# Kernel tuning notes

Measured on AMD Instinct MI355X. Metric: run time of the kernel, lower is better.

## Reference

```python
import jax, jax.numpy as jnp
import numpy as np

B, T = 1, 1024
V, C, H, L = 50304, 768, 12, 6
K = C // H              # 64, d_head
F = int(C * 3.5) // 32 * 32   # 2688, d_ffn
GN_EPS = 6.4e-4


def _layernorm(x, wb, eps=1e-5):
    mu = x.mean(-1, keepdims=True)
    var = jnp.var(x, axis=-1, keepdims=True)
    return (x - mu) * jax.lax.rsqrt(var + eps) * wb[0] + wb[1]


def _groupnorm(x, wb):  # x: [N, C], groups of size K per head
    xg = x.reshape(-1, H, K)
    mu = xg.mean(-1, keepdims=True)
    var = jnp.var(xg, axis=-1, keepdims=True)
    xg = (xg - mu) * jax.lax.rsqrt(var + GN_EPS)
    return xg.reshape(-1, C) * wb[0] + wb[1]


def _lerp(a, b, w):  # torch.lerp(a, b, w) = a + (b - a) * w
    return a + (b - a) * w


def _shift(x):  # token-shift with zero initial state (fresh LayerState)
    return jnp.concatenate([jnp.zeros_like(x[:, :1]), x[:, :-1]], axis=1)


def _layer(x, p):
    (tm_ln, tm_ts, Wr, Wk, Wv, Wg, Wo, bonus, decay, tm_gn,
     cm_ln, cm_ts, Win, Wout, cWg) = p
    # ---- time mixer ----
    xn = _layernorm(x, tm_ln)
    xp = _shift(xn)
    r = (_lerp(xp, xn, tm_ts[0]) @ Wr).reshape(B, T, H, K)
    k = (_lerp(xp, xn, tm_ts[1]) @ Wk).reshape(B, T, H, K)
    v = (_lerp(xp, xn, tm_ts[2]) @ Wv).reshape(B, T, H, K)
    g = _lerp(xp, xn, tm_ts[3]) @ Wg
    w = jnp.exp(-jnp.exp(decay))  # [H, K] per-channel decay

    def wkv_step(kv, rkv):  # kv: [B,H,K,V]
        r_t, k_t, v_t = rkv  # each [B,H,K]
        a = k_t[..., :, None] * v_t[..., None, :]          # outer product kv_t
        out = jnp.einsum('bhk,bhkv->bhv', r_t, kv + a * bonus[..., None])
        return kv * w[..., None] + a, out

    kv0 = jnp.zeros((B, H, K, K), x.dtype)
    kv_final, out = jax.lax.scan(
        wkv_step, kv0,
        (r.transpose(1, 0, 2, 3), k.transpose(1, 0, 2, 3),
         v.transpose(1, 0, 2, 3)))
    out = out.transpose(1, 0, 2, 3).reshape(B, T, C)
    out = _groupnorm(out.reshape(B * T, C), tm_gn).reshape(B, T, C)
    x = x + (out * jax.nn.silu(g)) @ Wo
    # ---- channel mixer ----
    xn = _layernorm(x, cm_ln)
    xp = _shift(xn)
    h = jnp.square(jax.nn.relu(_lerp(xp, xn, cm_ts[0]) @ Win))
    x = x + (h @ Wout) * jax.nn.sigmoid(_lerp(xp, xn, cm_ts[1]) @ cWg)
    return x, kv_final


def _forward(tokens, embed, embed_ln, tm_ln, tm_ts, tm_Wr, tm_Wk, tm_Wv,
             tm_Wg, tm_Wo, tm_bonus, tm_decay, tm_gn, cm_ln, cm_ts, cm_Win,
             cm_Wout, cm_Wg, head_ln, unembed):
    x = _layernorm(embed[tokens], embed_ln)
    stacked = (tm_ln, tm_ts, tm_Wr, tm_Wk, tm_Wv, tm_Wg, tm_Wo, tm_bonus,
               tm_decay, tm_gn, cm_ln, cm_ts, cm_Win, cm_Wout, cm_Wg)
    x, _ = jax.lax.scan(_layer, x, stacked)  # scan over the L layers
    return _layernorm(x, head_ln) @ unembed  # logits [B, T, V]


def setup_inputs() -> dict:
    key = jax.random.key(0)
    ks = iter(jax.random.split(key, 48))

    def rn(shape, s=0.02):
        return s * jax.random.normal(next(ks), shape, jnp.float32)

    def ln(pre=()):  # stacked (weight, bias) of a LayerNorm/GroupNorm
        return jnp.stack([1.0 + rn(pre + (C,)), rn(pre + (C,))], axis=len(pre))

    return {
        'tokens': jax.random.randint(next(ks), (B, T), 0, V),
        'embed': rn((V, C)),
        'embed_ln': ln(),
        'tm_ln': ln((L,)),
        'tm_ts': jax.random.uniform(next(ks), (L, 4, C), jnp.float32),
        'tm_Wr': rn((L, C, C)),
        'tm_Wk': rn((L, C, C)),
        'tm_Wv': rn((L, C, C)),
        'tm_Wg': rn((L, C, C)),
        'tm_Wo': rn((L, C, C)),
        'tm_bonus': rn((L, H, K), 0.5),
        'tm_decay': rn((L, H, K), 0.5),
        'tm_gn': ln((L,)),
        'cm_ln': ln((L,)),
        'cm_ts': jax.random.uniform(next(ks), (L, 2, C), jnp.float32),
        'cm_Win': rn((L, C, F)),
        'cm_Wout': rn((L, F, C)),
        'cm_Wg': rn((L, C, C)),
        'head_ln': ln(),
        'unembed': rn((C, V)),
    }


def reference(tokens, embed, embed_ln, tm_ln, tm_ts, tm_Wr, tm_Wk, tm_Wv,
              tm_Wg, tm_Wo, tm_bonus, tm_decay, tm_gn, cm_ln, cm_ts, cm_Win,
              cm_Wout, cm_Wg, head_ln, unembed):
    return _forward(tokens, embed, embed_ln, tm_ln, tm_ts, tm_Wr, tm_Wk,
                    tm_Wv, tm_Wg, tm_Wo, tm_bonus, tm_decay, tm_gn, cm_ln,
                    cm_ts, cm_Win, cm_Wout, cm_Wg, head_ln, unembed)
```

## Files before the change

kernel.cpp:

```cpp
#include <hip/hip_runtime.h>
#include <hip/hip_bf16.h>

#define T_LEN 1024
#define CDIM  768
#define HNUM  12
#define KDIM  64
#define LNUM  6
#define FDIM  2688
#define VDIM  50304
#define NCH   16
#define LCH   64

#define WSZ   (CDIM * CDIM)
#define WIN_OFF  (6 * WSZ)
#define WOUT_OFF (WIN_OFF + CDIM * FDIM)
#define WBUF_ELEMS (WOUT_OFF + FDIM * CDIM)

typedef __attribute__((ext_vector_type(4))) float f32x4;
typedef __attribute__((ext_vector_type(8))) short s16x8;

__device__ __forceinline__ ushort f2bf(float f) {
    union { float fv; unsigned u; } v; v.fv = f;
    unsigned r = v.u + 0x7fffu + ((v.u >> 16) & 1u);
    return (ushort)(r >> 16);
}

__device__ __forceinline__ void gload_lds16(const ushort* g, ushort* l) {
    __builtin_amdgcn_global_load_lds(
        (const __attribute__((address_space(1))) void*)g,
        (__attribute__((address_space(3))) void*)l, 16, 0, 0);
}

template <int N_>
__device__ __forceinline__ void wait_vm() {
    if constexpr (N_ == 0)      asm volatile("s_waitcnt vmcnt(0)" ::: "memory");
    else if constexpr (N_ == 4) asm volatile("s_waitcnt vmcnt(4)" ::: "memory");
    else if constexpr (N_ == 6) asm volatile("s_waitcnt vmcnt(6)" ::: "memory");
    else if constexpr (N_ == 8) asm volatile("s_waitcnt vmcnt(8)" ::: "memory");
    else                        asm volatile("s_waitcnt vmcnt(12)" ::: "memory");
}
__device__ __forceinline__ void barrier_asm() {
    asm volatile("s_barrier" ::: "memory");
}

__device__ __forceinline__ void trans_tile(const float* __restrict__ in,
        ushort* __restrict__ out, int R, int C, int tk, int tn) {
    __shared__ float tile[64][65];
    int tid = threadIdx.x;
    int r = tid >> 4, c4 = (tid & 15) << 2;
    int k0 = tk << 6, n0 = tn << 6;
    #pragma unroll
    for (int j = 0; j < 4; j++) {
        int rr = r + j * 16;
        float4 f = *(const float4*)&in[(size_t)(k0 + rr) * C + n0 + c4];
        tile[rr][c4 + 0] = f.x; tile[rr][c4 + 1] = f.y;
        tile[rr][c4 + 2] = f.z; tile[rr][c4 + 3] = f.w;
    }
    __syncthreads();
    #pragma unroll
    for (int j = 0; j < 4; j++) {
        int n = r + j * 16;
        ushort4 u;
        u.x = f2bf(tile[c4 + 0][n]);
        u.y = f2bf(tile[c4 + 1][n]);
        u.z = f2bf(tile[c4 + 2][n]);
        u.w = f2bf(tile[c4 + 3][n]);
        *(ushort4*)&out[(size_t)(n0 + n) * R + k0 + c4] = u;
    }
}

__global__ __launch_bounds__(256)
void k_trans(const float* __restrict__ in, ushort* __restrict__ out, int R, int C) {
    trans_tile(in, out, R, C, blockIdx.y, blockIdx.x);
}

__device__ __forceinline__ void conv_layer_tile(int t,
        const float* p0, const float* p1, const float* p2, const float* p3,
        const float* p4, const float* p5, const float* pWin, const float* pWout,
        ushort* wl) {
    const float* in; ushort* out; int R, C, tk, tn;
    if (t < 864) {
        int mi = t / 144, tt = t % 144;
        switch (mi) {
            case 0: in = p0; break; case 1: in = p1; break;
            case 2: in = p2; break; case 3: in = p3; break;
            case 4: in = p4; break; default: in = p5; break;
        }
        out = wl + (size_t)mi * WSZ; R = 768; C = 768;
        tk = tt / 12; tn = tt % 12;
    } else if (t < 1368) {
        int tt = t - 864;
        in = pWin; out = wl + WIN_OFF; R = 768; C = 2688;
        tk = tt / 42; tn = tt % 42;
    } else {
        int tt = t - 1368;
        in = pWout; out = wl + WOUT_OFF; R = 2688; C = 768;
        tk = tt / 12; tn = tt % 12;
    }
    trans_tile(in, out, R, C, tk, tn);
}

__global__ __launch_bounds__(256)
void k_conv_layer(const float* p0, const float* p1, const float* p2,
                  const float* p3, const float* p4, const float* p5,
                  const float* pWin, const float* pWout, ushort* wl) {
    conv_layer_tile(blockIdx.x, p0, p1, p2, p3, p4, p5, pWin, pWout, wl);
}

__global__ __launch_bounds__(256)
void k_conv_all(const float* Wr, const float* Wk, const float* Wv,
                const float* Wg, const float* Wo, const float* Wcg,
                const float* Win, const float* Wout, const float* unemb,
                ushort* wbuf, ushort* ubuf) {
    int b = blockIdx.x;
    if (b < 6 * 1872) {
        int l = b / 1872, t = b % 1872;
        conv_layer_tile(t,
            Wr + (size_t)l * WSZ, Wk + (size_t)l * WSZ, Wv + (size_t)l * WSZ,
            Wg + (size_t)l * WSZ, Wo + (size_t)l * WSZ, Wcg + (size_t)l * WSZ,
            Win + (size_t)l * CDIM * FDIM, Wout + (size_t)l * FDIM * CDIM,
            wbuf + (size_t)l * WBUF_ELEMS);
    } else {
        int t = b - 6 * 1872;
        int tk = t / 786, tn = t % 786;
        trans_tile(unemb, ubuf, CDIM, VDIM, tk, tn);
    }
}

__global__ __launch_bounds__(256)
void k_ln_bf(const float* __restrict__ x, const float* __restrict__ wb,
             ushort* __restrict__ out) {
    int t = blockIdx.x, tid = threadIdx.x;
    float v[3]; float s = 0.f, s2 = 0.f;
    #pragma unroll
    for (int j = 0; j < 3; j++) {
        v[j] = x[(size_t)t * CDIM + tid + j * 256];
        s += v[j]; s2 += v[j] * v[j];
    }
    #pragma unroll
    for (int m = 32; m; m >>= 1) { s += __shfl_xor(s, m); s2 += __shfl_xor(s2, m); }
    __shared__ float rs[4], rq[4];
    int w = tid >> 6;
    if ((tid & 63) == 0) { rs[w] = s; rq[w] = s2; }
    __syncthreads();
    s = rs[0] + rs[1] + rs[2] + rs[3];
    s2 = rq[0] + rq[1] + rq[2] + rq[3];
    float mu = s * (1.f / CDIM);
    float inv = rsqrtf(s2 * (1.f / CDIM) - mu * mu + 1e-5f);
    #pragma unroll
    for (int j = 0; j < 3; j++) {
        int c = tid + j * 256;
        out[(size_t)t * CDIM + c] = f2bf((v[j] - mu) * inv * wb[c] + wb[CDIM + c]);
    }
}

__global__ __launch_bounds__(256)
void k_embed_ln(const int* __restrict__ tok, const float* __restrict__ embed,
                const float* __restrict__ wb, float* __restrict__ xout) {
    int t = blockIdx.x, tid = threadIdx.x;
    const float* row = embed + (size_t)tok[t] * CDIM;
    float v[3]; float s = 0.f, s2 = 0.f;
    #pragma unroll
    for (int j = 0; j < 3; j++) {
        v[j] = row[tid + j * 256]; s += v[j]; s2 += v[j] * v[j];
    }
    #pragma unroll
    for (int m = 32; m; m >>= 1) { s += __shfl_xor(s, m); s2 += __shfl_xor(s2, m); }
    __shared__ float rs[4], rq[4];
    int w = tid >> 6;
    if ((tid & 63) == 0) { rs[w] = s; rq[w] = s2; }
    __syncthreads();
    s = rs[0] + rs[1] + rs[2] + rs[3];
    s2 = rq[0] + rq[1] + rq[2] + rq[3];
    float mu = s * (1.f / CDIM);
    float inv = rsqrtf(s2 * (1.f / CDIM) - mu * mu + 1e-5f);
    #pragma unroll
    for (int j = 0; j < 3; j++) {
        int c = tid + j * 256;
        xout[(size_t)t * CDIM + c] = (v[j] - mu) * inv * wb[c] + wb[CDIM + c];
    }
}

template <int NM>
__global__ __launch_bounds__(256)
void k_lnlerp(const float* __restrict__ x, const float* __restrict__ lnw,
              const float* __restrict__ ts, ushort* __restrict__ mix) {
    int t = blockIdx.x, tid = threadIdx.x;
    bool has = (t > 0);
    float vb[3], va[3];
    float sb = 0.f, qb = 0.f, sa = 0.f, qa = 0.f;
    #pragma unroll
    for (int j = 0; j < 3; j++) {
        int c = tid + j * 256;
        vb[j] = x[(size_t)t * CDIM + c];
        sb += vb[j]; qb += vb[j] * vb[j];
        va[j] = has ? x[(size_t)(t - 1) * CDIM + c] : 0.f;
        sa += va[j]; qa += va[j] * va[j];
    }
    #pragma unroll
    for (int m = 32; m; m >>= 1) {
        sb += __shfl_xor(sb, m); qb += __shfl_xor(qb, m);
        sa += __shfl_xor(sa, m); qa += __shfl_xor(qa, m);
    }
    __shared__ float r0[4], r1[4], r2[4], r3[4];
    int w = tid >> 6;
    if ((tid & 63) == 0) { r0[w] = sb; r1[w] = qb; r2[w] = sa; r3[w] = qa; }
    __syncthreads();
    sb = r0[0] + r0[1] + r0[2] + r0[3]; qb = r1[0] + r1[1] + r1[2] + r1[3];
    sa = r2[0] + r2[1] + r2[2] + r2[3]; qa = r3[0] + r3[1] + r3[2] + r3[3];
    float mub = sb * (1.f / CDIM);
    float invb = rsqrtf(qb * (1.f / CDIM) - mub * mub + 1e-5f);
    float mua = sa * (1.f / CDIM);
    float inva = rsqrtf(qa * (1.f / CDIM) - mua * mua + 1e-5f);
    #pragma unroll
    for (int j = 0; j < 3; j++) {
        int c = tid + j * 256;
        float wgt = lnw[c], bia = lnw[CDIM + c];
        float xb = (vb[j] - mub) * invb * wgt + bia;
        float xa = has ? (va[j] - mua) * inva * wgt + bia : 0.f;
        #pragma unroll
        for (int m = 0; m < NM; m++) {
            float tv = ts[m * CDIM + c];
            mix[((size_t)m * T_LEN + t) * CDIM + c] = f2bf(xa + (xb - xa) * tv);
        }
    }
}

template <int BM, int BN, int EPI>
__device__ __forceinline__ void gemm_body(
        const ushort* __restrict__ A, const ushort* __restrict__ Bt,
        float* __restrict__ Cf, ushort* __restrict__ Cb,
        const float* __restrict__ resid, const float* __restrict__ gate,
        int N, int K, int mb, int nb, ushort* Al, ushort* Bl) {
    const int tid = threadIdx.x, lane = tid & 63, wave = tid >> 6;
    constexpr int WM = BM / 2, WN = BN / 2, FM = WM / 16, FN = WN / 16;
    const int wm = (wave >> 1) * WM, wn = (wave & 1) * WN;
    constexpr int AR = (BM * 8) / 256;
    constexpr int BR = (BN * 8) / 256;
    constexpr int LD = AR + BR;

    auto stage = [&](int buf, int kt) {
        int k0 = kt << 6;
        #pragma unroll
        for (int r = 0; r < AR; r++) {
            int slot = tid + r * 256;
            int row = slot >> 3, g = slot & 7;
            int gk = ((g ^ (row & 7)) << 3);
            gload_lds16(A + (size_t)(mb + row) * K + k0 + gk,
                        &Al[buf * BM * 64 + slot * 8]);
        }
        #pragma unroll
        for (int r = 0; r < BR; r++) {
            int slot = tid + r * 256;
            int row = slot >> 3, g = slot & 7;
            int gk = ((g ^ (row & 7)) << 3);
            gload_lds16(Bt + (size_t)(nb + row) * K + k0 + gk,
                        &Bl[buf * BN * 64 + slot * 8]);
        }
    };

    f32x4 acc[FM][FN];
    #pragma unroll
    for (int i = 0; i < FM; i++)
        #pragma unroll
        for (int j = 0; j < FN; j++) acc[i][j] = (f32x4)0.f;

    const int nt = K >> 6;
    stage(0, 0);
    stage(1, 1);
    int cur = 0;
    for (int t = 0; t < nt; t++) {
        if (t + 1 < nt) wait_vm<LD>();
        else            wait_vm<0>();
        barrier_asm();
        const ushort* Ab = &Al[cur * BM * 64];
        const ushort* Bb = &Bl[cur * BN * 64];
        const int kq = lane >> 4, ln15 = lane & 15;
        #pragma unroll
        for (int s = 0; s < 2; s++) {
            s16x8 af[FM], bfr[FN];
            #pragma unroll
            for (int i = 0; i < FM; i++) {
                int row = wm + i * 16 + ln15;
                int g = (s * 4 + kq) ^ (row & 7);
                af[i] = *(const s16x8*)&Ab[row * 64 + g * 8];
            }
            #pragma unroll
            for (int j = 0; j < FN; j++) {
                int row = wn + j * 16 + ln15;
                int g = (s * 4 + kq) ^ (row & 7);
                bfr[j] = *(const s16x8*)&Bb[row * 64 + g * 8];
            }
            #pragma unroll
            for (int i = 0; i < FM; i++)
                #pragma unroll
                for (int j = 0; j < FN; j++)
                    acc[i][j] = __builtin_amdgcn_mfma_f32_16x16x32_bf16(
                        af[i], bfr[j], acc[i][j], 0, 0, 0);
        }
        barrier_asm();
        if (t + 2 < nt) stage(cur, t + 2);
        cur ^= 1;
    }
    #pragma unroll
    for (int i = 0; i < FM; i++) {
        int rbase = mb + wm + i * 16 + (lane >> 4) * 4;
        #pragma unroll
        for (int j = 0; j < FN; j++) {
            int col = nb + wn + j * 16 + (lane & 15);
            #pragma unroll
            for (int r = 0; r < 4; r++) {
                size_t idx = (size_t)(rbase + r) * N + col;
                float vv = acc[i][j][r];
                if constexpr (EPI == 0) {
                    Cf[idx] = vv;
                } else if constexpr (EPI == 1) {
                    Cf[idx] = resid[idx] + vv;
                } else if constexpr (EPI == 2) {
                    float z = vv > 0.f ? vv * vv : 0.f;
                    Cb[idx] = f2bf(z);
                } else {
                    float gv = gate[idx];
                    Cf[idx] = resid[idx] + vv / (1.f + __expf(-gv));
                }
            }
        }
    }
}

template <int BM, int BN, int EPI, bool BATCH>
__global__ __launch_bounds__(256)
void k_gemm_std(const ushort* __restrict__ A, const ushort* __restrict__ Bt,
                float* __restrict__ Cf, ushort* __restrict__ Cb,
                const float* __restrict__ resid, const float* __restrict__ gate,
                int N, int K) {
    __shared__ __align__(16) ushort Al[2 * BM * 64];
    __shared__ __align__(16) ushort Bl[2 * BN * 64];
    if constexpr (BATCH) {
        int z = blockIdx.z;
        A  += (size_t)z * T_LEN * CDIM;
        Bt += (size_t)z * CDIM * CDIM;
        Cf += (size_t)z * T_LEN * CDIM;
    }
    gemm_body<BM, BN, EPI>(A, Bt, Cf, Cb, resid, gate, N, K,
                           blockIdx.y * BM, blockIdx.x * BN, Al, Bl);
}

__global__ __launch_bounds__(256)
void k_gemm_head(const ushort* __restrict__ A, const ushort* __restrict__ Bt,
                 float* __restrict__ C) {
    __shared__ __align__(16) ushort Al[2 * 128 * 64];
    __shared__ __align__(16) ushort Bl[2 * 128 * 64];
    int id = blockIdx.x;
    int xcd = id & 7, slot = id >> 3;
    int mb = slot & 7, nbl = slot >> 3;
    int nb = nbl * 8 + xcd;
    if (nb >= VDIM / 128) return;
    gemm_body<128, 128, 0>(A, Bt, C, nullptr, nullptr, nullptr,
                           VDIM, CDIM, mb * 128, nb * 128, Al, Bl);
}

__global__ __launch_bounds__(256)
void k_cmix(const ushort* __restrict__ mix, const ushort* __restrict__ wl,
            ushort* __restrict__ hb, float* __restrict__ gcm) {
    __shared__ __align__(16) ushort Al[2 * 128 * 64];
    __shared__ __align__(16) ushort Bl[2 * 64 * 64];
    int bx = blockIdx.x, mb = blockIdx.y * 128;
    if (bx < FDIM / 64) {
        gemm_body<128, 64, 2>(mix, wl + WIN_OFF, nullptr, hb, nullptr, nullptr,
                              FDIM, CDIM, mb, bx * 64, Al, Bl);
    } else {
        gemm_body<128, 64, 0>(mix + (size_t)T_LEN * CDIM, wl + 5 * WSZ, gcm,
                              nullptr, nullptr, nullptr, CDIM, CDIM, mb,
                              (bx - FDIM / 64) * 64, Al, Bl);
    }
}

__global__ __launch_bounds__(256)
void k_wkv1(const float* __restrict__ kb, const float* __restrict__ vb,
            const float* __restrict__ decay, float* __restrict__ Stil) {
    int c = blockIdx.x / HNUM, h = blockIdx.x % HNUM;
    __shared__ float kl[4096], vl[4096], wsh[64];
    int tid = threadIdx.x;
    for (int idx = tid; idx < 4096; idx += 256) {
        int j = idx >> 6, cc = idx & 63;
        size_t g = (size_t)(c * LCH + j) * CDIM + h * 64 + cc;
        kl[idx] = kb[g]; vl[idx] = vb[g];
    }
    if (tid < 64) wsh[tid] = expf(-expf(decay[h * 64 + tid]));
    __syncthreads();
    int k = tid >> 2, v0 = (tid & 3) * 16;
    float w = wsh[k], f = 1.f;
    float s[16];
    #pragma unroll
    for (int i = 0; i < 16; i++) s[i] = 0.f;
    for (int j = 63; j >= 0; --j) {
        float kw = kl[j * 64 + k] * f;
        #pragma unroll
        for (int i = 0; i < 16; i++) s[i] += kw * vl[j * 64 + v0 + i];
        f *= w;
    }
    float* dst = Stil + ((size_t)(c * HNUM + h) << 12) + k * 64 + v0;
    #pragma unroll
    for (int i = 0; i < 16; i++) dst[i] = s[i];
}

__global__ __launch_bounds__(256)
void k_wkv23(const float* __restrict__ rb, const float* __restrict__ kb,
             const float* __restrict__ vb, const float* __restrict__ Stil,
             const float* __restrict__ decay, const float* __restrict__ bonus,
             const float* __restrict__ gate, const float* __restrict__ gnw,
             ushort* __restrict__ y) {
    int c = blockIdx.x / HNUM, h = blockIdx.x % HNUM;
    __shared__ float rl[4096], kl[4096], vl[4096];
    __shared__ float part[4][4096];
    __shared__ float wsh[64], bsh[64];
    int tid = threadIdx.x;
    for (int idx = tid; idx < 4096; idx += 256) {
        int j = idx >> 6, cc = idx & 63;
        size_t g = (size_t)(c * LCH + j) * CDIM + h * 64 + cc;
        rl[idx] = rb[g]; kl[idx] = kb[g]; vl[idx] = vb[g];
    }
    if (tid < 64) {
        wsh[tid] = expf(-expf(decay[h * 64 + tid]));
        bsh[tid] = bonus[h * 64 + tid];
    }
    __syncthreads();
    int v = tid & 63, kg = tid >> 6;
    float S[16], wr[16], br[16], w64[16];
    #pragma unroll
    for (int i = 0; i < 16; i++) {
        S[i] = 0.f;
        wr[i] = wsh[kg * 16 + i];
        br[i] = bsh[kg * 16 + i];
        float e = expf(decay[h * 64 + kg * 16 + i]);
        w64[i] = expf(-64.f * e);
    }
    for (int cc = 0; cc < c; cc++) {
        const float* sp = Stil + ((size_t)(cc * HNUM + h) << 12);
        #pragma unroll
        for (int i = 0; i < 16; i++)
            S[i] = S[i] * w64[i] + sp[(kg * 16 + i) * 64 + v];
    }
    for (int j = 0; j < 64; j++) {
        float vj = vl[j * 64 + v];
        const float4* kp = (const float4*)&kl[j * 64 + kg * 16];
        const float4* rp = (const float4*)&rl[j * 64 + kg * 16];
        float rsum = 0.f;
        #pragma unroll
        for (int q = 0; q < 4; q++) {
            float4 k4 = kp[q], r4 = rp[q];
            const float* kf = (const float*)&k4;
            const float* rf = (const float*)&r4;
            #pragma unroll
            for (int e = 0; e < 4; e++) {
                int i = q * 4 + e;
                float a = kf[e] * vj;
                rsum += rf[e] * (S[i] + a * br[i]);
                S[i] = S[i] * wr[i] + a;
            }
        }
        part[kg][j * 64 + v] = rsum;
    }
    __syncthreads();
    for (int jj = 0; jj < 16; jj++) {
        int j = kg * 16 + jj;
        float o = part[0][j * 64 + v] + part[1][j * 64 + v] +
                  part[2][j * 64 + v] + part[3][j * 64 + v];
        float s = o, s2 = o * o;
        #pragma unroll
        for (int m = 32; m; m >>= 1) { s += __shfl_xor(s, m); s2 += __shfl_xor(s2, m); }
        float mu = s * (1.f / 64.f);
        float var = s2 * (1.f / 64.f) - mu * mu;
        float xg = (o - mu) * rsqrtf(var + 6.4e-4f);
        int t = c * LCH + j, col = h * 64 + v;
        float gv = gate[(size_t)t * CDIM + col];
        float silu = gv / (1.f + __expf(-gv));
        y[(size_t)t * CDIM + col] = f2bf((xg * gnw[col] + gnw[CDIM + col]) * silu);
    }
}

extern "C" void kernel_launch(void* const* d_in, const int* in_sizes, int n_in,
                              void* d_out, int out_size, void* d_ws, size_t ws_size,
                              hipStream_t stream) {
    const int*   tok      = (const int*)d_in[0];
    const float* embed    = (const float*)d_in[1];
    const float* embed_ln = (const float*)d_in[2];
    const float* tm_ln    = (const float*)d_in[3];
    const float* tm_ts    = (const float*)d_in[4];
    const float* tm_Wr    = (const float*)d_in[5];
    const float* tm_Wk    = (const float*)d_in[6];
    const float* tm_Wv    = (const float*)d_in[7];
    const float* tm_Wg    = (const float*)d_in[8];
    const float* tm_Wo    = (const float*)d_in[9];
    const float* tm_bonus = (const float*)d_in[10];
    const float* tm_decay = (const float*)d_in[11];
    const float* tm_gn    = (const float*)d_in[12];
    const float* cm_ln    = (const float*)d_in[13];
    const float* cm_ts    = (const float*)d_in[14];
    const float* cm_Win   = (const float*)d_in[15];
    const float* cm_Wout  = (const float*)d_in[16];
    const float* cm_Wg    = (const float*)d_in[17];
    const float* head_ln  = (const float*)d_in[18];
    const float* unembed  = (const float*)d_in[19];
    float* out = (float*)d_out;

    const size_t TC = (size_t)T_LEN * CDIM;
    char* wp = (char*)d_ws;
    auto alloc = [&](size_t bytes) {
        char* p = wp; wp += (bytes + 255) & ~(size_t)255; return p;
    };
    float*  x    = (float*)alloc(TC * 4);
    ushort* mix  = (ushort*)alloc(4 * TC * 2);
    float*  rkvg = (float*)alloc(4 * TC * 4);
    float*  gcm  = (float*)alloc(TC * 4);
    ushort* y    = (ushort*)alloc(TC * 2);
    ushort* hb   = (ushort*)alloc((size_t)T_LEN * FDIM * 2);
    float*  Stil = (float*)alloc((size_t)NCH * HNUM * 4096 * 4);
    ushort* ubuf = (ushort*)alloc((size_t)CDIM * VDIM * 2);
    size_t fixed_bytes = (size_t)(wp - (char*)d_ws);
    const size_t per_layer = ((size_t)WBUF_ELEMS * 2 + 255) & ~(size_t)255;
    bool all6 = (fixed_bytes + 6 * per_layer) <= ws_size;
    ushort* wbuf = (ushort*)alloc(all6 ? 6 * per_layer : per_layer);
    if ((size_t)(wp - (char*)d_ws) > ws_size) return;

    if (all6) {
        k_conv_all<<<6 * 1872 + 9432, 256, 0, stream>>>(
            tm_Wr, tm_Wk, tm_Wv, tm_Wg, tm_Wo, cm_Wg, cm_Win, cm_Wout,
            unembed, wbuf, ubuf);
    } else {
        k_trans<<<dim3(VDIM / 64, CDIM / 64), 256, 0, stream>>>(
            unembed, ubuf, CDIM, VDIM);
    }
    k_embed_ln<<<T_LEN, 256, 0, stream>>>(tok, embed, embed_ln, x);

    dim3 g64(CDIM / 64, T_LEN / 64);
    dim3 gQKVG(CDIM / 64, T_LEN / 128, 4);
    dim3 gCmix(FDIM / 64 + CDIM / 64, T_LEN / 128);

    for (int l = 0; l < LNUM; l++) {
        ushort* wl = all6 ? (ushort*)((char*)wbuf + (size_t)l * per_layer) : wbuf;
        if (!all6) {
            const size_t lo = (size_t)l * CDIM * CDIM;
            k_conv_layer<<<1872, 256, 0, stream>>>(
                tm_Wr + lo, tm_Wk + lo, tm_Wv + lo, tm_Wg + lo, tm_Wo + lo,
                cm_Wg + lo, cm_Win + (size_t)l * CDIM * FDIM,
                cm_Wout + (size_t)l * FDIM * CDIM, wl);
        }
        const float* dec = tm_decay + (size_t)l * HNUM * KDIM;
        const float* bon = tm_bonus + (size_t)l * HNUM * KDIM;

        k_lnlerp<4><<<T_LEN, 256, 0, stream>>>(x, tm_ln + (size_t)l * 2 * CDIM,
                                               tm_ts + (size_t)l * 4 * CDIM, mix);
        k_gemm_std<128,64,0,true><<<gQKVG, 256, 0, stream>>>(
            mix, wl, rkvg, nullptr, nullptr, nullptr, CDIM, CDIM);
        k_wkv1<<<NCH * HNUM, 256, 0, stream>>>(rkvg + TC, rkvg + 2 * TC, dec, Stil);
        k_wkv23<<<NCH * HNUM, 256, 0, stream>>>(rkvg, rkvg + TC, rkvg + 2 * TC,
            Stil, dec, bon, rkvg + 3 * TC, tm_gn + (size_t)l * 2 * CDIM, y);
        k_gemm_std<64,64,1,false><<<g64, 256, 0, stream>>>(
            y, wl + 4 * WSZ, x, nullptr, x, nullptr, CDIM, CDIM);

        k_lnlerp<2><<<T_LEN, 256, 0, stream>>>(x, cm_ln + (size_t)l * 2 * CDIM,
                                               cm_ts + (size_t)l * 2 * CDIM, mix);
        k_cmix<<<gCmix, 256, 0, stream>>>(mix, wl, hb, gcm);
        k_gemm_std<64,64,3,false><<<g64, 256, 0, stream>>>(
            hb, wl + WOUT_OFF, x, nullptr, x, gcm, CDIM, FDIM);
    }

    k_ln_bf<<<T_LEN, 256, 0, stream>>>(x, head_ln, mix);
    k_gemm_head<<<3200, 256, 0, stream>>>(mix, ubuf, out);
}
```

Baseline: 966.0 us.

## Replace head GEMM with 256x256-tile 512-thread kernel over zero-padded unembedding

Swaps the 128x128 vocab-projection GEMM for a new kernel with 256x256 tiles, 8 waves, 128 KB of dynamic LDS with double buffering, XOR-swizzled LDS layout, setprio around the MFMA bursts, and nontemporal output stores. The transposed unembedding buffer is zero-padded to a multiple of 256 so the last tile loads without bounds checks, and work is remapped across XCDs. The goal is more operand reuse per tile and less global traffic for the large head GEMM. In exchange occupancy drops to about one block per CU, and there is only 788 blocks of work to spread over the device.

```diff
diff --git a/kernel.cpp b/kernel.cpp
--- a/kernel.cpp
+++ b/kernel.cpp
@@ -8,6 +8,7 @@
 #define LNUM  6
 #define FDIM  2688
 #define VDIM  50304
+#define NPAD  50432
 #define NCH   16
 #define LCH   64
 
@@ -72,6 +73,14 @@
 __global__ __launch_bounds__(256)
 void k_trans(const float* __restrict__ in, ushort* __restrict__ out, int R, int C) {
     trans_tile(in, out, R, C, blockIdx.y, blockIdx.x);
+}
+
+__global__ __launch_bounds__(256)
+void k_padzero(ushort* __restrict__ ubuf) {
+    size_t base = (size_t)VDIM * CDIM;
+    for (int i = threadIdx.x + blockIdx.x * 256; i < (NPAD - VDIM) * CDIM;
+         i += 256 * gridDim.x)
+        ubuf[base + i] = 0;
 }
 
 __device__ __forceinline__ void conv_layer_tile(int t,
@@ -122,8 +131,14 @@
             wbuf + (size_t)l * WBUF_ELEMS);
     } else {
         int t = b - 6 * 1872;
-        int tk = t / 786, tn = t % 786;
-        trans_tile(unemb, ubuf, CDIM, VDIM, tk, tn);
+        if (t < 9432) {
+            int tk = t / 786, tn = t % 786;
+            trans_tile(unemb, ubuf, CDIM, VDIM, tk, tn);
+        } else {
+            size_t base = (size_t)VDIM * CDIM;
+            for (int i = threadIdx.x; i < (NPAD - VDIM) * CDIM; i += 256)
+                ubuf[base + i] = 0;
+        }
     }
 }
 
@@ -346,18 +361,104 @@
                            blockIdx.y * BM, blockIdx.x * BN, Al, Bl);
 }
 
-__global__ __launch_bounds__(256)
-void k_gemm_head(const ushort* __restrict__ A, const ushort* __restrict__ Bt,
-                 float* __restrict__ C) {
-    __shared__ __align__(16) ushort Al[2 * 128 * 64];
-    __shared__ __align__(16) ushort Bl[2 * 128 * 64];
-    int id = blockIdx.x;
-    int xcd = id & 7, slot = id >> 3;
-    int mb = slot & 7, nbl = slot >> 3;
-    int nb = nbl * 8 + xcd;
-    if (nb >= VDIM / 128) return;
-    gemm_body<128, 128, 0>(A, Bt, C, nullptr, nullptr, nullptr,
-                           VDIM, CDIM, mb * 128, nb * 128, Al, Bl);
+__global__ __launch_bounds__(512)
+void k_head256(const ushort* __restrict__ A, const ushort* __restrict__ Bt,
+               float* __restrict__ C) {
+    extern __shared__ __align__(16) ushort lds[];
+    ushort* Al = lds;
+    ushort* Bl = lds + 2 * 16384;
+    const int tid = threadIdx.x, lane = tid & 63, wave = tid >> 6;
+    const int total = gridDim.x;
+    int q = total >> 3, r = total & 7;
+    int xcd = blockIdx.x & 7, loc = blockIdx.x >> 3;
+    int work = (xcd < r ? xcd * (q + 1) : r * (q + 1) + (xcd - r) * q) + loc;
+    const int nbase = (work >> 2) * 256, mbase = (work & 3) * 256;
+    const int wm = (wave >> 2) * 128, wn = (wave & 3) * 64;
+
+    auto stage = [&](int buf, int kt) {
+        int k0 = kt << 6;
+        #pragma unroll
+        for (int rr = 0; rr < 4; rr++) {
+            int slot = tid + rr * 512;
+            int row = slot >> 3, g = slot & 7;
+            int gk = ((g ^ (row & 7)) << 3);
+            gload_lds16(A + (size_t)(mbase + row) * CDIM + k0 + gk,
+                        &Al[buf * 16384 + slot * 8]);
+        }
+        #pragma unroll
+        for (int rr = 0; rr < 4; rr++) {
+            int slot = tid + rr * 512;
+            int row = slot >> 3, g = slot & 7;
+            int gk = ((g ^ (row & 7)) << 3);
+            gload_lds16(Bt + (size_t)(nbase + row) * CDIM + k0 + gk,
+                        &Bl[buf * 16384 + slot * 8]);
+        }
+    };
+
+    f32x4 acc[8][4];
+    #pragma unroll
+    for (int i = 0; i < 8; i++)
+        #pragma unroll
+        for (int j = 0; j < 4; j++) acc[i][j] = (f32x4)0.f;
+
+    const int kq = lane >> 4, ln15 = lane & 15;
+    stage(0, 0);
+    stage(1, 1);
+    int cur = 0;
+    for (int t = 0; t < 12; t++) {
+        if (t < 11) wait_vm<8>();
+        else        wait_vm<0>();
+        barrier_asm();
+        const ushort* Ab = &Al[cur * 16384];
+        const ushort* Bb = &Bl[cur * 16384];
+        #pragma unroll
+        for (int ks = 0; ks < 2; ks++) {
+            s16x8 bfr[4];
+            #pragma unroll
+            for (int j = 0; j < 4; j++) {
+                int row = wn + j * 16 + ln15;
+                int g = (ks * 4 + kq) ^ (row & 7);
+                bfr[j] = *(const s16x8*)&Bb[row * 64 + g * 8];
+            }
+            #pragma unroll
+            for (int mh = 0; mh < 2; mh++) {
+                s16x8 af[4];
+                #pragma unroll
+                for (int i = 0; i < 4; i++) {
+                    int row = wm + mh * 64 + i * 16 + ln15;
+                    int g = (ks * 4 + kq) ^ (row & 7);
+                    af[i] = *(const s16x8*)&Ab[row * 64 + g * 8];
+                }
+                asm volatile("s_waitcnt lgkmcnt(0)" ::: "memory");
+                __builtin_amdgcn_sched_barrier(0);
+                __builtin_amdgcn_s_setprio(1);
+                #pragma unroll
+                for (int i = 0; i < 4; i++)
+                    #pragma unroll
+                    for (int j = 0; j < 4; j++)
+                        acc[mh * 4 + i][j] = __builtin_amdgcn_mfma_f32_16x16x32_bf16(
+                            af[i], bfr[j], acc[mh * 4 + i][j], 0, 0, 0);
+                __builtin_amdgcn_s_setprio(0);
+            }
+        }
+        barrier_asm();
+        if (t + 2 < 12) stage(cur, t + 2);
+        cur ^= 1;
+    }
+    #pragma unroll
+    for (int a = 0; a < 8; a++) {
+        int rbase = mbase + wm + (a >> 2) * 64 + (a & 3) * 16 + (lane >> 4) * 4;
+        #pragma unroll
+        for (int j = 0; j < 4; j++) {
+            int col = nbase + wn + j * 16 + ln15;
+            if (col < VDIM) {
+                #pragma unroll
+                for (int rr = 0; rr < 4; rr++)
+                    __builtin_nontemporal_store(acc[a][j][rr],
+                        &C[(size_t)(rbase + rr) * VDIM + col]);
+            }
+        }
+    }
 }
 
 __global__ __launch_bounds__(256)
@@ -448,13 +549,13 @@
         const float4* rp = (const float4*)&rl[j * 64 + kg * 16];
         float rsum = 0.f;
         #pragma unroll
-        for (int q = 0; q < 4; q++) {
-            float4 k4 = kp[q], r4 = rp[q];
+        for (int qq = 0; qq < 4; qq++) {
+            float4 k4 = kp[qq], r4 = rp[qq];
             const float* kf = (const float*)&k4;
             const float* rf = (const float*)&r4;
             #pragma unroll
             for (int e = 0; e < 4; e++) {
-                int i = q * 4 + e;
+                int i = qq * 4 + e;
                 float a = kf[e] * vj;
                 rsum += rf[e] * (S[i] + a * br[i]);
                 S[i] = S[i] * wr[i] + a;
@@ -517,20 +618,24 @@
     ushort* y    = (ushort*)alloc(TC * 2);
     ushort* hb   = (ushort*)alloc((size_t)T_LEN * FDIM * 2);
     float*  Stil = (float*)alloc((size_t)NCH * HNUM * 4096 * 4);
-    ushort* ubuf = (ushort*)alloc((size_t)CDIM * VDIM * 2);
+    ushort* ubuf = (ushort*)alloc((size_t)NPAD * CDIM * 2);
     size_t fixed_bytes = (size_t)(wp - (char*)d_ws);
     const size_t per_layer = ((size_t)WBUF_ELEMS * 2 + 255) & ~(size_t)255;
     bool all6 = (fixed_bytes + 6 * per_layer) <= ws_size;
     ushort* wbuf = (ushort*)alloc(all6 ? 6 * per_layer : per_layer);
     if ((size_t)(wp - (char*)d_ws) > ws_size) return;
 
+    (void)hipFuncSetAttribute((const void*)k_head256,
+            hipFuncAttributeMaxDynamicSharedMemorySize, 131072);
+
     if (all6) {
-        k_conv_all<<<6 * 1872 + 9432, 256, 0, stream>>>(
+        k_conv_all<<<6 * 1872 + 9432 + 1, 256, 0, stream>>>(
             tm_Wr, tm_Wk, tm_Wv, tm_Wg, tm_Wo, cm_Wg, cm_Win, cm_Wout,
             unembed, wbuf, ubuf);
     } else {
         k_trans<<<dim3(VDIM / 64, CDIM / 64), 256, 0, stream>>>(
             unembed, ubuf, CDIM, VDIM);
+        k_padzero<<<8, 256, 0, stream>>>(ubuf);
     }
     k_embed_ln<<<T_LEN, 256, 0, stream>>>(tok, embed, embed_ln, x);
 
@@ -568,5 +673,5 @@
     }
 
     k_ln_bf<<<T_LEN, 256, 0, stream>>>(x, head_ln, mix);
-    k_gemm_head<<<3200, 256, 0, stream>>>(mix, ubuf, out);
-}
+    k_head256<<<788, 512, 131072, stream>>>(mix, ubuf, out);
+}
```

New measurement: 954.9 us. About the same (-1.1%).

## Fuse chunked WKV state and output kernels with inter-block flag synchronisation

Applied to the files above, without the earlier changes.

Merges the two WKV kernels (per-chunk state computation and the scan/output pass) into one launch. Each block writes its chunk state, then publishes it through a release-store flag tagged with the layer generation. Later chunks spin on acquire loads of earlier chunks' flags before accumulating their states. This drops one launch per layer and the reload of k/v into shared memory, and w^64 is now computed by repeated squaring instead of expf. The cost is a busy-wait that depends on all 192 blocks being co-resident to avoid deadlock, plus an extra memset.

```diff
diff --git a/kernel.cpp b/kernel.cpp
--- a/kernel.cpp
+++ b/kernel.cpp
@@ -377,48 +377,20 @@
 }
 
 __global__ __launch_bounds__(256)
-void k_wkv1(const float* __restrict__ kb, const float* __restrict__ vb,
-            const float* __restrict__ decay, float* __restrict__ Stil) {
-    int c = blockIdx.x / HNUM, h = blockIdx.x % HNUM;
-    __shared__ float kl[4096], vl[4096], wsh[64];
-    int tid = threadIdx.x;
-    for (int idx = tid; idx < 4096; idx += 256) {
-        int j = idx >> 6, cc = idx & 63;
-        size_t g = (size_t)(c * LCH + j) * CDIM + h * 64 + cc;
-        kl[idx] = kb[g]; vl[idx] = vb[g];
-    }
-    if (tid < 64) wsh[tid] = expf(-expf(decay[h * 64 + tid]));
-    __syncthreads();
-    int k = tid >> 2, v0 = (tid & 3) * 16;
-    float w = wsh[k], f = 1.f;
-    float s[16];
-    #pragma unroll
-    for (int i = 0; i < 16; i++) s[i] = 0.f;
-    for (int j = 63; j >= 0; --j) {
-        float kw = kl[j * 64 + k] * f;
-        #pragma unroll
-        for (int i = 0; i < 16; i++) s[i] += kw * vl[j * 64 + v0 + i];
-        f *= w;
-    }
-    float* dst = Stil + ((size_t)(c * HNUM + h) << 12) + k * 64 + v0;
-    #pragma unroll
-    for (int i = 0; i < 16; i++) dst[i] = s[i];
-}
-
-__global__ __launch_bounds__(256)
-void k_wkv23(const float* __restrict__ rb, const float* __restrict__ kb,
-             const float* __restrict__ vb, const float* __restrict__ Stil,
-             const float* __restrict__ decay, const float* __restrict__ bonus,
-             const float* __restrict__ gate, const float* __restrict__ gnw,
-             ushort* __restrict__ y) {
+void k_wkv(const float* __restrict__ rb, const float* __restrict__ kb,
+           const float* __restrict__ vb, float* __restrict__ Stil,
+           int* __restrict__ flags, int gen,
+           const float* __restrict__ decay, const float* __restrict__ bonus,
+           const float* __restrict__ gate, const float* __restrict__ gnw,
+           ushort* __restrict__ y) {
     int c = blockIdx.x / HNUM, h = blockIdx.x % HNUM;
     __shared__ float rl[4096], kl[4096], vl[4096];
     __shared__ float part[4][4096];
     __shared__ float wsh[64], bsh[64];
     int tid = threadIdx.x;
     for (int idx = tid; idx < 4096; idx += 256) {
-        int j = idx >> 6, cc = idx & 63;
-        size_t g = (size_t)(c * LCH + j) * CDIM + h * 64 + cc;
+        int j = idx >> 6, cc2 = idx & 63;
+        size_t g = (size_t)(c * LCH + j) * CDIM + h * 64 + cc2;
         rl[idx] = rb[g]; kl[idx] = kb[g]; vl[idx] = vb[g];
     }
     if (tid < 64) {
@@ -426,6 +398,27 @@
         bsh[tid] = bonus[h * 64 + tid];
     }
     __syncthreads();
+    {
+        int k = tid >> 2, v0 = (tid & 3) * 16;
+        float w = wsh[k], f = 1.f;
+        float s[16];
+        #pragma unroll
+        for (int i = 0; i < 16; i++) s[i] = 0.f;
+        for (int j = 63; j >= 0; --j) {
+            float kw = kl[j * 64 + k] * f;
+            #pragma unroll
+            for (int i = 0; i < 16; i++) s[i] += kw * vl[j * 64 + v0 + i];
+            f *= w;
+        }
+        float* dst = Stil + ((size_t)(c * HNUM + h) << 12) + k * 64 + v0;
+        #pragma unroll
+        for (int i = 0; i < 16; i++) dst[i] = s[i];
+    }
+    __threadfence();
+    __syncthreads();
+    if (tid == 0)
+        __hip_atomic_store(&flags[c * HNUM + h], gen, __ATOMIC_RELEASE,
+                           __HIP_MEMORY_SCOPE_AGENT);
     int v = tid & 63, kg = tid >> 6;
     float S[16], wr[16], br[16], w64[16];
     #pragma unroll
@@ -433,10 +426,16 @@
         S[i] = 0.f;
         wr[i] = wsh[kg * 16 + i];
         br[i] = bsh[kg * 16 + i];
-        float e = expf(decay[h * 64 + kg * 16 + i]);
-        w64[i] = expf(-64.f * e);
+        float t2 = wr[i];
+        t2 *= t2; t2 *= t2; t2 *= t2; t2 *= t2; t2 *= t2; t2 *= t2;
+        w64[i] = t2;
     }
     for (int cc = 0; cc < c; cc++) {
+        if (tid == 0) {
+            while (__hip_atomic_load(&flags[cc * HNUM + h], __ATOMIC_ACQUIRE,
+                                     __HIP_MEMORY_SCOPE_AGENT) < gen) {}
+        }
+        __syncthreads();
         const float* sp = Stil + ((size_t)(cc * HNUM + h) << 12);
         #pragma unroll
         for (int i = 0; i < 16; i++)
@@ -448,13 +447,13 @@
         const float4* rp = (const float4*)&rl[j * 64 + kg * 16];
         float rsum = 0.f;
         #pragma unroll
-        for (int q = 0; q < 4; q++) {
-            float4 k4 = kp[q], r4 = rp[q];
+        for (int qq = 0; qq < 4; qq++) {
+            float4 k4 = kp[qq], r4 = rp[qq];
             const float* kf = (const float*)&k4;
             const float* rf = (const float*)&r4;
             #pragma unroll
             for (int e = 0; e < 4; e++) {
-                int i = q * 4 + e;
+                int i = qq * 4 + e;
                 float a = kf[e] * vj;
                 rsum += rf[e] * (S[i] + a * br[i]);
                 S[i] = S[i] * wr[i] + a;
@@ -517,12 +516,15 @@
     ushort* y    = (ushort*)alloc(TC * 2);
     ushort* hb   = (ushort*)alloc((size_t)T_LEN * FDIM * 2);
     float*  Stil = (float*)alloc((size_t)NCH * HNUM * 4096 * 4);
+    int*    flags= (int*)alloc(NCH * HNUM * 4);
     ushort* ubuf = (ushort*)alloc((size_t)CDIM * VDIM * 2);
     size_t fixed_bytes = (size_t)(wp - (char*)d_ws);
     const size_t per_layer = ((size_t)WBUF_ELEMS * 2 + 255) & ~(size_t)255;
     bool all6 = (fixed_bytes + 6 * per_layer) <= ws_size;
     ushort* wbuf = (ushort*)alloc(all6 ? 6 * per_layer : per_layer);
     if ((size_t)(wp - (char*)d_ws) > ws_size) return;
+
+    hipMemsetAsync(flags, 0, NCH * HNUM * 4, stream);
 
     if (all6) {
         k_conv_all<<<6 * 1872 + 9432, 256, 0, stream>>>(
@@ -554,9 +556,9 @@
                                                tm_ts + (size_t)l * 4 * CDIM, mix);
         k_gemm_std<128,64,0,true><<<gQKVG, 256, 0, stream>>>(
             mix, wl, rkvg, nullptr, nullptr, nullptr, CDIM, CDIM);
-        k_wkv1<<<NCH * HNUM, 256, 0, stream>>>(rkvg + TC, rkvg + 2 * TC, dec, Stil);
-        k_wkv23<<<NCH * HNUM, 256, 0, stream>>>(rkvg, rkvg + TC, rkvg + 2 * TC,
-            Stil, dec, bon, rkvg + 3 * TC, tm_gn + (size_t)l * 2 * CDIM, y);
+        k_wkv<<<NCH * HNUM, 256, 0, stream>>>(rkvg, rkvg + TC, rkvg + 2 * TC,
+            Stil, flags, l + 1, dec, bon, rkvg + 3 * TC,
+            tm_gn + (size_t)l * 2 * CDIM, y);
         k_gemm_std<64,64,1,false><<<g64, 256, 0, stream>>>(
             y, wl + 4 * WSZ, x, nullptr, x, nullptr, CDIM, CDIM);
 
```

After: 1.195 ms. +23.7%, slower.
